# Kernel tuning notes

Hardware: AMD Instinct MI355X
Metric: run time of the kernel (lower is better)

Reference implementation:

```python
import jax, jax.numpy as jnp
import numpy as np

NUM_HEADS = 16
HEAD_DIM = 64
PATCH_NUMS = [1, 2, 3, 4, 5, 6, 8, 10, 13, 16, 32]
MAX_SCALE_MUL = float(np.log(100.0))


def precompute_freqs_cis(dim, patch_nums, theta=10000.0):
    # Returns [L, dim//2, 2] (cos, sin) pairs; matches torch.polar construction.
    freqs = 1.0 / theta ** (np.arange(0, dim, 4)[: dim // 4].astype(np.float32) / dim)  # [dim//4]
    tx, ty = [], []
    grid = 32.0
    for p in patch_nums:
        ix, iy = np.meshgrid(np.arange(p), np.arange(p), indexing="ij")  # torch default 'ij'
        tx.append(ix.flatten().astype(np.float32) / p * grid)
        ty.append(iy.flatten().astype(np.float32) / p * grid)
    tx = np.concatenate(tx)
    ty = np.concatenate(ty)
    ang = np.concatenate([np.outer(tx, freqs), np.outer(ty, freqs)], axis=1).astype(np.float32)  # [L, dim//2]
    return np.stack([np.cos(ang), np.sin(ang)], axis=-1)  # [L, dim//2, 2]


FREQS_CIS_CROSS = jnp.asarray(precompute_freqs_cis(HEAD_DIM, [12]))  # [144, 32, 2]


def _rope(x, cis):
    # x: [B, H, S, D]; cis: [S, D//2, 2] -> complex multiply on (even, odd) pairs.
    B, H, S, D = x.shape
    xr = x.reshape(B, H, S, D // 2, 2)
    a, b = xr[..., 0], xr[..., 1]
    c = cis[..., 0][None, None]  # [1,1,S,D//2]
    d = cis[..., 1][None, None]
    return jnp.stack([a * c - b * d, a * d + b * c], axis=-1).reshape(B, H, S, D)


def setup_inputs() -> dict:
    key = jax.random.key(0)
    ks = jax.random.split(key, 6)
    B, C, Ck, Lk = 8, 1024, 1024, 144
    fc = precompute_freqs_cis(HEAD_DIM, PATCH_NUMS)
    L = fc.shape[0]  # 1704
    return {
        "x": jax.random.normal(ks[0], (B, L, C), jnp.float32),
        "y": jax.random.normal(ks[1], (B, Lk, Ck), jnp.float32),
        "freqs_cis": jnp.asarray(fc),
        "attn_bias": jax.random.normal(ks[2], (1, 1, L, Lk), jnp.float32) * 0.1,
        "Wq": jax.random.normal(ks[3], (C, C), jnp.float32) * 0.02,
        "q_bias": jnp.zeros((C,), jnp.float32),
        "Wkv": jax.random.normal(ks[4], (2 * C, Ck), jnp.float32) * 0.02,
        "v_bias": jnp.zeros((C,), jnp.float32),
        "Wproj": jax.random.normal(ks[5], (C, C), jnp.float32) * 0.02,
        "b_proj": jnp.zeros((C,), jnp.float32),
        "scale_mul": jnp.full((1, NUM_HEADS, 1, 1), np.log(4.0), jnp.float32),
    }


def reference(x, y, freqs_cis, attn_bias, Wq, q_bias, Wkv, v_bias, Wproj, b_proj, scale_mul):
    B, L, C = x.shape
    H, D = NUM_HEADS, HEAD_DIM
    Lk = y.shape[1]
    # fused QKV projections (k bias is the zero buffer)
    q = (x @ Wq.T + q_bias).reshape(B, L, H, D).transpose(0, 2, 1, 3)  # [B,H,L,D]
    kv_bias = jnp.concatenate([jnp.zeros_like(v_bias), v_bias])
    kv = (y @ Wkv.T + kv_bias).reshape(B, Lk, 2, H, D)
    k = kv[:, :, 0].transpose(0, 2, 1, 3)  # [B,H,Lk,D]
    v = kv[:, :, 1].transpose(0, 2, 1, 3)
    # attn_l2_norm path: scale = 1, per-head learned multiplier
    sm = jnp.exp(jnp.minimum(scale_mul, MAX_SCALE_MUL))  # [1,H,1,1]
    q = q / jnp.maximum(jnp.linalg.norm(q, axis=-1, keepdims=True), 1e-12) * sm
    k = k / jnp.maximum(jnp.linalg.norm(k, axis=-1, keepdims=True), 1e-12)
    # inline RoPE (cross freqs recomputed from 12x12 grid every forward in the original)
    q = _rope(q, freqs_cis)
    k = _rope(k, FREQS_CIS_CROSS)
    # manual (non-flash) masked attention, scale = 1 due to l2 norm
    logits = jnp.einsum("bhld,bhkd->bhlk", q, k) + attn_bias
    attn = jax.nn.softmax(logits, axis=-1)
    oup = jnp.einsum("bhlk,bhkd->bhld", attn, v).transpose(0, 2, 1, 3).reshape(B, L, C)
    return oup @ Wproj.T + b_proj
```

## Files before the change

### kernel.cpp

```cpp
#include <hip/hip_runtime.h>

using u16 = unsigned short;
using u32 = unsigned int;

typedef __bf16 bf16x8 __attribute__((ext_vector_type(8)));
typedef float  f32x4  __attribute__((ext_vector_type(4)));
typedef _Float16 f16;
typedef _Float16 f16x4 __attribute__((ext_vector_type(4)));
typedef _Float16 f16x8 __attribute__((ext_vector_type(8)));
typedef u16 u16x4 __attribute__((ext_vector_type(4)));

__device__ __forceinline__ float b2f(u16 u) { return __uint_as_float(((u32)u) << 16); }
__device__ __forceinline__ u16 f2b(float f) {
    u32 u = __float_as_uint(f);
    return (u16)((u + 0x7FFFu + ((u >> 16) & 1u)) >> 16);
}

__device__ __forceinline__ void async_cp16(void* lds, const void* g) {
    __builtin_amdgcn_global_load_lds(
        (const __attribute__((address_space(1))) u32*)g,
        (__attribute__((address_space(3))) u32*)lds, 16, 0, 0);
}

__device__ __forceinline__ void split4_store(const float* src, u16* hi, u16* lo, int i) {
    f32x4 v = reinterpret_cast<const f32x4*>(src)[i];
    u16x4 H, L;
#pragma unroll
    for (int j = 0; j < 4; j++) {
        u16 hb = f2b(v[j]);
        H[j] = hb;
        L[j] = f2b(v[j] - b2f(hb));
    }
    reinterpret_cast<u16x4*>(hi)[i] = H;
    reinterpret_cast<u16x4*>(lo)[i] = L;
}

__global__ __launch_bounds__(256) void prep(const float* __restrict__ x,
                                            const float* __restrict__ Wq,
                                            const float* __restrict__ Wp,
                                            u16* __restrict__ xhi, u16* __restrict__ xlo,
                                            u16* __restrict__ wqhi, u16* __restrict__ wqlo,
                                            f16* __restrict__ wph,
                                            int nx4, int nw4) {
    int i = blockIdx.x * 256 + threadIdx.x;
    if (i < nx4) {
        split4_store(x, xhi, xlo, i);
    } else if (i < nx4 + nw4) {
        split4_store(Wq, wqhi, wqlo, i - nx4);
    } else {
        int k = i - nx4 - nw4;
        if (k < nw4) {
            f32x4 v = reinterpret_cast<const f32x4*>(Wp)[k];
            f16x4 h = {(f16)v[0], (f16)v[1], (f16)v[2], (f16)v[3]};
            reinterpret_cast<f16x4*>(wph)[k] = h;
        }
    }
}

__device__ __forceinline__ void split8(f32x4 a0, f32x4 a1, bf16x8& hi, bf16x8& lo) {
    union { bf16x8 v; u16 s[8]; } H, L;
#pragma unroll
    for (int j = 0; j < 4; j++) {
        float f = a0[j]; u16 hb = f2b(f); H.s[j] = hb;     L.s[j] = f2b(f - b2f(hb));
        float g = a1[j]; u16 gb = f2b(g); H.s[4 + j] = gb; L.s[4 + j] = f2b(g - b2f(gb));
    }
    hi = H.v; lo = L.v;
}

__global__ __launch_bounds__(256) void gemm_q(const u16* __restrict__ xhi,
                                              const u16* __restrict__ xlo,
                                              const u16* __restrict__ whi,
                                              const u16* __restrict__ wlo,
                                              const float* __restrict__ qb,
                                              const float* __restrict__ fc,
                                              const float* __restrict__ smul,
                                              f16* __restrict__ qout) {
    const int K = 1024, L = 1704;
    __shared__ u16 xs[2][2][64][64];
    int tid = threadIdx.x;
    int lane = tid & 63, wv = tid >> 6;
    int mt = blockIdx.x >> 2;
    int hg = blockIdx.x & 3;
    int h  = hg * 4 + wv;
    int lr = lane & 15, quad = lane >> 4;
    long m0 = (long)mt * 64;

    int r0 = tid >> 3, c0 = tid & 7;
    int s1 = tid + 256;
    int r1 = s1 >> 3, c1 = s1 & 7;
    const u16* srch0 = xhi + (m0 + r0) * K + ((c0 ^ (r0 & 7)) * 8);
    const u16* srch1 = xhi + (m0 + r1) * K + ((c1 ^ (r1 & 7)) * 8);
    const u16* srcl0 = xlo + (m0 + r0) * K + ((c0 ^ (r0 & 7)) * 8);
    const u16* srcl1 = xlo + (m0 + r1) * K + ((c1 ^ (r1 & 7)) * 8);
    u16* dh[2][2]; u16* dl[2][2];
    dh[0][0] = &xs[0][0][r0][c0 * 8]; dh[0][1] = &xs[0][0][r1][c1 * 8];
    dh[1][0] = &xs[1][0][r0][c0 * 8]; dh[1][1] = &xs[1][0][r1][c1 * 8];
    dl[0][0] = &xs[0][1][r0][c0 * 8]; dl[0][1] = &xs[0][1][r1][c1 * 8];
    dl[1][0] = &xs[1][1][r0][c0 * 8]; dl[1][1] = &xs[1][1][r1][c1 * 8];

    const bf16x8* wh_p[4];
    const bf16x8* wl_p[4];
#pragma unroll
    for (int i = 0; i < 4; i++) {
        long woff = ((long)(h * 64 + i * 16 + lr)) * K;
        wh_p[i] = reinterpret_cast<const bf16x8*>(whi + woff) + quad;
        wl_p[i] = reinterpret_cast<const bf16x8*>(wlo + woff) + quad;
    }

    int sp0 = ((0 + quad) ^ (lr & 7)) * 8;
    int sp1 = ((4 + quad) ^ (lr & 7)) * 8;

    f32x4 acc[4][4] = {};

    async_cp16(dh[0][0], srch0); async_cp16(dh[0][1], srch1);
    async_cp16(dl[0][0], srcl0); async_cp16(dl[0][1], srcl1);
    __syncthreads();

    for (int c = 0; c < 16; c++) {
        if (c < 15) {
            int nb = (c + 1) & 1;
            int off = (c + 1) * 64;
            async_cp16(dh[nb][0], srch0 + off); async_cp16(dh[nb][1], srch1 + off);
            async_cp16(dl[nb][0], srcl0 + off); async_cp16(dl[nb][1], srcl1 + off);
        }
        int buf = c & 1;
#pragma unroll
        for (int s = 0; s < 2; s++) {
            int sp = s ? sp1 : sp0;
            bf16x8 AH[4], AL[4], WH[4], WL[4];
#pragma unroll
            for (int i = 0; i < 4; i++) {
                WH[i] = wh_p[i][c * 8 + s * 4];
                WL[i] = wl_p[i][c * 8 + s * 4];
            }
#pragma unroll
            for (int i = 0; i < 4; i++) {
                AH[i] = *reinterpret_cast<const bf16x8*>(&xs[buf][0][i * 16 + lr][sp]);
                AL[i] = *reinterpret_cast<const bf16x8*>(&xs[buf][1][i * 16 + lr][sp]);
            }
#pragma unroll
            for (int mi = 0; mi < 4; mi++)
#pragma unroll
                for (int ni = 0; ni < 4; ni++) {
                    acc[mi][ni] = __builtin_amdgcn_mfma_f32_16x16x32_bf16(AH[mi], WH[ni], acc[mi][ni], 0, 0, 0);
                    acc[mi][ni] = __builtin_amdgcn_mfma_f32_16x16x32_bf16(AL[mi], WH[ni], acc[mi][ni], 0, 0, 0);
                    acc[mi][ni] = __builtin_amdgcn_mfma_f32_16x16x32_bf16(AH[mi], WL[ni], acc[mi][ni], 0, 0, 0);
                }
        }
        __syncthreads();
    }

    float sm = __expf(fminf(smul[h], 4.6051702f));
#pragma unroll
    for (int mi = 0; mi < 4; mi++) {
#pragma unroll
        for (int r = 0; r < 4; r++) {
            long rowg = m0 + mi * 16 + quad * 4 + r;
            float v[4];
            float ss = 0.f;
#pragma unroll
            for (int ni = 0; ni < 4; ni++) {
                v[ni] = acc[mi][ni][r] + qb[h * 64 + ni * 16 + lr];
                ss += v[ni] * v[ni];
            }
            ss += __shfl_xor(ss, 1, 64); ss += __shfl_xor(ss, 2, 64);
            ss += __shfl_xor(ss, 4, 64); ss += __shfl_xor(ss, 8, 64);
            float inv = sm / fmaxf(sqrtf(ss), 1e-12f);
            int l = (int)(rowg % L);
            f16* orow = qout + rowg * 1024 + h * 64;
#pragma unroll
            for (int ni = 0; ni < 4; ni++) {
                float u = v[ni] * inv;
                int d = ni * 16 + lr;
                int j = d >> 1;
                float c = fc[(l * 32 + j) * 2];
                float s = fc[(l * 32 + j) * 2 + 1];
                float pr = __shfl_xor(u, 1, 64);
                float o = (lane & 1) ? (pr * s + u * c) : (u * c - pr * s);
                orow[d] = (f16)o;
            }
        }
    }
}

__constant__ double FREQS16[16] = {
    1.0, 0.5623413251903491, 0.31622776601683794, 0.17782794100389228,
    0.1, 0.05623413251903491, 0.03162277660168379, 0.017782794100389228,
    0.01, 0.005623413251903491, 0.0031622776601683794, 0.0017782794100389228,
    0.001, 0.0005623413251903491, 0.00031622776601683794, 0.00017782794100389228};

__global__ __launch_bounds__(256) void gemm_kv(const float* __restrict__ y,
                                               const float* __restrict__ Wkv,
                                               const float* __restrict__ vb,
                                               f16* __restrict__ khp,
                                               f16* __restrict__ klp,
                                               f16* __restrict__ vhp,
                                               f16* __restrict__ vlp) {
    const int K = 1024;
    int lane = threadIdx.x & 63, wv = threadIdx.x >> 6;
    int mt = blockIdx.x >> 3;
    int nt = (blockIdx.x & 7) * 4 + wv;
    int lr = lane & 15, quad = lane >> 4;
    long m0 = (long)mt * 64;

    const float* arow[4];
    const float* wrow[4];
#pragma unroll
    for (int i = 0; i < 4; i++) {
        arow[i] = y   + (m0 + i * 16 + lr) * K + quad * 8;
        wrow[i] = Wkv + ((long)(nt * 64 + i * 16 + lr)) * K + quad * 8;
    }

    f32x4 acc[4][4] = {};
    for (int ks = 0; ks < 32; ks++) {
        bf16x8 ah[4], al[4], wh[4], wl[4];
#pragma unroll
        for (int i = 0; i < 4; i++) {
            const float* ap = arow[i] + ks * 32;
            split8(*(const f32x4*)ap, *(const f32x4*)(ap + 4), ah[i], al[i]);
            const float* wp = wrow[i] + ks * 32;
            split8(*(const f32x4*)wp, *(const f32x4*)(wp + 4), wh[i], wl[i]);
        }
#pragma unroll
        for (int mi = 0; mi < 4; mi++)
#pragma unroll
            for (int ni = 0; ni < 4; ni++) {
                acc[mi][ni] = __builtin_amdgcn_mfma_f32_16x16x32_bf16(ah[mi], wh[ni], acc[mi][ni], 0, 0, 0);
                acc[mi][ni] = __builtin_amdgcn_mfma_f32_16x16x32_bf16(al[mi], wh[ni], acc[mi][ni], 0, 0, 0);
                acc[mi][ni] = __builtin_amdgcn_mfma_f32_16x16x32_bf16(ah[mi], wl[ni], acc[mi][ni], 0, 0, 0);
            }
    }

    bool isv = nt >= 16;
    int h = isv ? nt - 16 : nt;
#pragma unroll
    for (int mi = 0; mi < 4; mi++) {
#pragma unroll
        for (int r = 0; r < 4; r++) {
            long row = m0 + mi * 16 + quad * 4 + r;
            int b = (int)(row / 144), lk = (int)(row % 144);
            long bh = b * 16 + h;
            float v[4];
#pragma unroll
            for (int ni = 0; ni < 4; ni++)
                v[ni] = acc[mi][ni][r] + (isv ? vb[h * 64 + ni * 16 + lr] : 0.f);
            if (!isv) {
                float ss = v[0] * v[0] + v[1] * v[1] + v[2] * v[2] + v[3] * v[3];
                ss += __shfl_xor(ss, 1, 64); ss += __shfl_xor(ss, 2, 64);
                ss += __shfl_xor(ss, 4, 64); ss += __shfl_xor(ss, 8, 64);
                float inv = 1.f / fmaxf(sqrtf(ss), 1e-12f);
                f16* kh_row = khp + (bh * 144 + lk) * 64;
                f16* kl_row = klp + (bh * 144 + lk) * 64;
#pragma unroll
                for (int ni = 0; ni < 4; ni++) {
                    float u = v[ni] * inv;
                    int d = ni * 16 + lr;
                    int j = d >> 1;
                    int f = j & 15;
                    float tc = (j < 16) ? ((float)(lk / 12)) / 12.0f * 32.0f
                                        : ((float)(lk % 12)) / 12.0f * 32.0f;
                    float ang = (float)((double)tc * FREQS16[f]);
                    float c = cosf(ang), s = sinf(ang);
                    float pr = __shfl_xor(u, 1, 64);
                    float o = (lane & 1) ? (pr * s + u * c) : (u * c - pr * s);
                    f16 oh = (f16)o;
                    f16 ol = (f16)(o - (float)oh);
                    kh_row[d] = oh;
                    kl_row[d] = ol;
                }
            } else {
#pragma unroll
                for (int ni = 0; ni < 4; ni++) {
                    float val = v[ni];
                    int d = ni * 16 + lr;
                    f16 vh = (f16)val;
                    f16 vl = (f16)(val - (float)vh);
                    vhp[(bh * 64 + d) * 144 + lk] = vh;
                    vlp[(bh * 64 + d) * 144 + lk] = vl;
                }
            }
        }
    }
}

__global__ __launch_bounds__(256, 3) void attn(const f16* q,
                                               const f16* __restrict__ khp,
                                               const f16* __restrict__ klp,
                                               const f16* __restrict__ vhp,
                                               const f16* __restrict__ vlp,
                                               const float* __restrict__ abias,
                                               f16* aout) {
    const int L = 1704;
    __shared__ __align__(16) f16 ps[4][16][152];
    int tid = threadIdx.x;
    int lane = tid & 63, wv = tid >> 6;
    int lr = lane & 15, quad = lane >> 4;
    int ltile = blockIdx.x % 27;
    int bh = blockIdx.x / 27;
    int h = bh & 15, b = bh >> 4;
    int l0 = ltile * 64;
    int rows = min(64, L - l0);

    int rA = wv * 16 + lr;
    int rAc = min(rA, rows - 1);
    const f16* qrow = q + ((long)(b * L + l0 + rAc)) * 1024 + h * 64;
    f16x8 qa0 = *reinterpret_cast<const f16x8*>(qrow + quad * 8);
    f16x8 qa1 = *reinterpret_cast<const f16x8*>(qrow + 32 + quad * 8);

    const f16* khb = khp + (long)bh * (144 * 64);
    const f16* klb = klp + (long)bh * (144 * 64);

    f32x4 acc[9] = {};
#pragma unroll
    for (int t = 0; t < 9; t++) {
        const f16* k0 = khb + (t * 16 + lr) * 64 + quad * 8;
        const f16* k1 = klb + (t * 16 + lr) * 64 + quad * 8;
        f16x8 bh0 = *reinterpret_cast<const f16x8*>(k0);
        f16x8 bh1 = *reinterpret_cast<const f16x8*>(k0 + 32);
        f16x8 bl0 = *reinterpret_cast<const f16x8*>(k1);
        f16x8 bl1 = *reinterpret_cast<const f16x8*>(k1 + 32);
        acc[t] = __builtin_amdgcn_mfma_f32_16x16x32_f16(qa0, bh0, acc[t], 0, 0, 0);
        acc[t] = __builtin_amdgcn_mfma_f32_16x16x32_f16(qa1, bh1, acc[t], 0, 0, 0);
        acc[t] = __builtin_amdgcn_mfma_f32_16x16x32_f16(qa0, bl0, acc[t], 0, 0, 0);
        acc[t] = __builtin_amdgcn_mfma_f32_16x16x32_f16(qa1, bl1, acc[t], 0, 0, 0);
    }

    int rC = wv * 16 + quad * 4;
#pragma unroll
    for (int r = 0; r < 4; r++) {
        long lrow = (long)(l0 + min(rC + r, rows - 1)) * 144;
#pragma unroll
        for (int t = 0; t < 9; t++) acc[t][r] += abias[lrow + t * 16 + lr];
    }

#pragma unroll
    for (int r = 0; r < 4; r++) {
        float mx = acc[0][r];
#pragma unroll
        for (int t = 1; t < 9; t++) mx = fmaxf(mx, acc[t][r]);
        mx = fmaxf(mx, __shfl_xor(mx, 1, 64));
        mx = fmaxf(mx, __shfl_xor(mx, 2, 64));
        mx = fmaxf(mx, __shfl_xor(mx, 4, 64));
        mx = fmaxf(mx, __shfl_xor(mx, 8, 64));
        float s = 0.f;
#pragma unroll
        for (int t = 0; t < 9; t++) {
            float e = __expf(acc[t][r] - mx);
            acc[t][r] = e;
            s += e;
        }
        s += __shfl_xor(s, 1, 64);
        s += __shfl_xor(s, 2, 64);
        s += __shfl_xor(s, 4, 64);
        s += __shfl_xor(s, 8, 64);
        float inv = 1.0f / s;
#pragma unroll
        for (int t = 0; t < 9; t++)
            ps[wv][quad * 4 + r][t * 16 + lr] = (f16)(acc[t][r] * inv);
    }

    const f16* vhb = vhp + (long)bh * (64 * 144);
    const f16* vlb = vlp + (long)bh * (64 * 144);
    f32x4 oacc[4] = {};
#pragma unroll
    for (int ks = 0; ks < 5; ks++) {
        f16x8 pa = {0, 0, 0, 0, 0, 0, 0, 0};
        if (ks < 4 || quad < 2)
            pa = *reinterpret_cast<const f16x8*>(&ps[wv][lr][ks * 32 + quad * 8]);
#pragma unroll
        for (int n = 0; n < 4; n++) {
            f16x8 vh8 = {0, 0, 0, 0, 0, 0, 0, 0};
            f16x8 vl8 = {0, 0, 0, 0, 0, 0, 0, 0};
            if (ks < 4 || quad < 2) {
                const f16* vr  = vhb + (n * 16 + lr) * 144 + ks * 32 + quad * 8;
                const f16* vr2 = vlb + (n * 16 + lr) * 144 + ks * 32 + quad * 8;
                vh8 = *reinterpret_cast<const f16x8*>(vr);
                vl8 = *reinterpret_cast<const f16x8*>(vr2);
            }
            oacc[n] = __builtin_amdgcn_mfma_f32_16x16x32_f16(pa, vh8, oacc[n], 0, 0, 0);
            oacc[n] = __builtin_amdgcn_mfma_f32_16x16x32_f16(pa, vl8, oacc[n], 0, 0, 0);
        }
    }

    long ob = (long)(b * L + l0);
#pragma unroll
    for (int r = 0; r < 4; r++) {
        int rw = rC + r;
        if (rw < rows) {
            f16* ao = aout + (ob + rw) * 1024 + h * 64;
#pragma unroll
            for (int n = 0; n < 4; n++) ao[n * 16 + lr] = (f16)oacc[n][r];
        }
    }
}

__global__ __launch_bounds__(256) void gemm_proj(const f16* __restrict__ A,
                                                 const f16* __restrict__ Wh,
                                                 const float* __restrict__ bias,
                                                 float* __restrict__ out) {
    const int K = 1024;
    __shared__ f16 as[2][64][64];
    int tid = threadIdx.x;
    int lane = tid & 63, wv = tid >> 6;
    int mt = blockIdx.x >> 2;
    int cg = blockIdx.x & 3;
    int lr = lane & 15, quad = lane >> 4;
    long m0 = (long)mt * 64;
    long n0 = (long)cg * 256 + wv * 64;

    int r0 = tid >> 3, c0 = tid & 7;
    int s1i = tid + 256;
    int r1 = s1i >> 3, c1 = s1i & 7;
    const f16* srca0 = A + (m0 + r0) * K + ((c0 ^ (r0 & 7)) * 8);
    const f16* srca1 = A + (m0 + r1) * K + ((c1 ^ (r1 & 7)) * 8);
    f16* da[2][2];
    da[0][0] = &as[0][r0][c0 * 8]; da[0][1] = &as[0][r1][c1 * 8];
    da[1][0] = &as[1][r0][c0 * 8]; da[1][1] = &as[1][r1][c1 * 8];

    const f16x8* wrow[4];
#pragma unroll
    for (int i = 0; i < 4; i++)
        wrow[i] = reinterpret_cast<const f16x8*>(Wh + (n0 + i * 16 + lr) * K) + quad;

    int sp0 = ((0 + quad) ^ (lr & 7)) * 8;
    int sp1 = ((4 + quad) ^ (lr & 7)) * 8;

    f32x4 acc[4][4] = {};

    async_cp16(da[0][0], srca0);
    async_cp16(da[0][1], srca1);
    __syncthreads();

    for (int c = 0; c < 16; c++) {
        if (c < 15) {
            int nb = (c + 1) & 1;
            int off = (c + 1) * 64;
            async_cp16(da[nb][0], srca0 + off);
            async_cp16(da[nb][1], srca1 + off);
        }
        int buf = c & 1;
#pragma unroll
        for (int s = 0; s < 2; s++) {
            int sp = s ? sp1 : sp0;
            f16x8 af[4], wf[4];
#pragma unroll
            for (int i = 0; i < 4; i++) wf[i] = wrow[i][c * 8 + s * 4];
#pragma unroll
            for (int i = 0; i < 4; i++)
                af[i] = *reinterpret_cast<const f16x8*>(&as[buf][i * 16 + lr][sp]);
#pragma unroll
            for (int mi = 0; mi < 4; mi++)
#pragma unroll
                for (int ni = 0; ni < 4; ni++)
                    acc[mi][ni] = __builtin_amdgcn_mfma_f32_16x16x32_f16(af[mi], wf[ni], acc[mi][ni], 0, 0, 0);
        }
        __syncthreads();
    }

#pragma unroll
    for (int ni = 0; ni < 4; ni++) {
        int col = (int)n0 + ni * 16 + lr;
        float b = bias[col];
#pragma unroll
        for (int mi = 0; mi < 4; mi++) {
            long row = m0 + mi * 16 + quad * 4;
#pragma unroll
            for (int r = 0; r < 4; r++)
                out[(row + r) * 1024 + col] = acc[mi][ni][r] + b;
        }
    }
}

extern "C" void kernel_launch(void* const* d_in, const int* in_sizes, int n_in,
                              void* d_out, int out_size, void* d_ws, size_t ws_size,
                              hipStream_t stream) {
    const float* x     = (const float*)d_in[0];
    const float* y     = (const float*)d_in[1];
    const float* fc    = (const float*)d_in[2];
    const float* abias = (const float*)d_in[3];
    const float* Wq    = (const float*)d_in[4];
    const float* qb    = (const float*)d_in[5];
    const float* Wkv   = (const float*)d_in[6];
    const float* vb    = (const float*)d_in[7];
    const float* Wp    = (const float*)d_in[8];
    const float* bp    = (const float*)d_in[9];
    const float* smul  = (const float*)d_in[10];

    const long XN = 13959168L;
    const long WN = 1048576L;
    const long KVN = 1179648L;

    f16* qbuf  = (f16*)d_ws;
    u16* wq_hi = (u16*)(qbuf + XN);
    u16* wq_lo = wq_hi + WN;
    f16* wp_h  = (f16*)(wq_lo + WN);

    u16* x_hi = (u16*)d_out;
    u16* x_lo = x_hi + XN;
    f16* kh_p  = (f16*)d_out;
    f16* kl_p  = kh_p + KVN;
    f16* vth_p = kl_p + KVN;
    f16* vtl_p = vth_p + KVN;

    int nx4 = (int)(XN / 4);
    int nw4 = (int)(WN / 4);
    int prep_blocks = (nx4 + 2 * nw4) / 256;

    prep<<<dim3(prep_blocks), dim3(256), 0, stream>>>(x, Wq, Wp, x_hi, x_lo,
                                                      wq_hi, wq_lo, wp_h, nx4, nw4);
    gemm_q<<<dim3(852), dim3(256), 0, stream>>>(x_hi, x_lo, wq_hi, wq_lo, qb, fc, smul, qbuf);
    gemm_kv<<<dim3(144), dim3(256), 0, stream>>>(y, Wkv, vb, kh_p, kl_p, vth_p, vtl_p);
    attn<<<dim3(3456), dim3(256), 0, stream>>>(qbuf, kh_p, kl_p, vth_p, vtl_p, abias, (f16*)qbuf);
    gemm_proj<<<dim3(852), dim3(256), 0, stream>>>((const f16*)qbuf, wp_h, bp, (float*)d_out);
}
```

Baseline: 586.2 us.

## Drop LDS staging in Q and proj GEMMs, load operands directly, remap blocks

Both GEMM kernels stop staging the activation tile through shared memory with async copies and barriers. Each wave now loads its A fragments straight from global memory, just like the weight fragments. Block indices are remapped so that groups of 8 consecutive M-tiles share a head or column group, which should help L2 reuse. Launch bounds also add occupancy hints (3 and 4 blocks). Without LDS, the 4 waves of a block load the same A rows redundantly, so the kernels depend more on cache hits and global latency and lose the double-buffered prefetch.

```diff
diff --git a/kernel.cpp b/kernel.cpp
--- a/kernel.cpp
+++ b/kernel.cpp
@@ -14,12 +14,6 @@
 __device__ __forceinline__ u16 f2b(float f) {
     u32 u = __float_as_uint(f);
     return (u16)((u + 0x7FFFu + ((u >> 16) & 1u)) >> 16);
-}
-
-__device__ __forceinline__ void async_cp16(void* lds, const void* g) {
-    __builtin_amdgcn_global_load_lds(
-        (const __attribute__((address_space(1))) u32*)g,
-        (__attribute__((address_space(3))) u32*)lds, 16, 0, 0);
 }
 
 __device__ __forceinline__ void split4_store(const float* src, u16* hi, u16* lo, int i) {
@@ -67,76 +61,62 @@
     hi = H.v; lo = L.v;
 }
 
-__global__ __launch_bounds__(256) void gemm_q(const u16* __restrict__ xhi,
-                                              const u16* __restrict__ xlo,
-                                              const u16* __restrict__ whi,
-                                              const u16* __restrict__ wlo,
-                                              const float* __restrict__ qb,
-                                              const float* __restrict__ fc,
-                                              const float* __restrict__ smul,
-                                              f16* __restrict__ qout) {
+__device__ __forceinline__ void remap852(int j, int& mt, int& sg) {
+    if (j < 832) {
+        int a = j >> 5, rem = j & 31;
+        mt = a * 8 + (rem & 7);
+        sg = rem >> 3;
+    } else {
+        int rem = j - 832;
+        mt = 208 + rem % 5;
+        sg = rem / 5;
+    }
+}
+
+__global__ __launch_bounds__(256, 3) void gemm_q(const u16* __restrict__ xhi,
+                                                 const u16* __restrict__ xlo,
+                                                 const u16* __restrict__ whi,
+                                                 const u16* __restrict__ wlo,
+                                                 const float* __restrict__ qb,
+                                                 const float* __restrict__ fc,
+                                                 const float* __restrict__ smul,
+                                                 f16* __restrict__ qout) {
     const int K = 1024, L = 1704;
-    __shared__ u16 xs[2][2][64][64];
     int tid = threadIdx.x;
     int lane = tid & 63, wv = tid >> 6;
-    int mt = blockIdx.x >> 2;
-    int hg = blockIdx.x & 3;
+    int mt, hg;
+    remap852(blockIdx.x, mt, hg);
     int h  = hg * 4 + wv;
     int lr = lane & 15, quad = lane >> 4;
     long m0 = (long)mt * 64;
 
-    int r0 = tid >> 3, c0 = tid & 7;
-    int s1 = tid + 256;
-    int r1 = s1 >> 3, c1 = s1 & 7;
-    const u16* srch0 = xhi + (m0 + r0) * K + ((c0 ^ (r0 & 7)) * 8);
-    const u16* srch1 = xhi + (m0 + r1) * K + ((c1 ^ (r1 & 7)) * 8);
-    const u16* srcl0 = xlo + (m0 + r0) * K + ((c0 ^ (r0 & 7)) * 8);
-    const u16* srcl1 = xlo + (m0 + r1) * K + ((c1 ^ (r1 & 7)) * 8);
-    u16* dh[2][2]; u16* dl[2][2];
-    dh[0][0] = &xs[0][0][r0][c0 * 8]; dh[0][1] = &xs[0][0][r1][c1 * 8];
-    dh[1][0] = &xs[1][0][r0][c0 * 8]; dh[1][1] = &xs[1][0][r1][c1 * 8];
-    dl[0][0] = &xs[0][1][r0][c0 * 8]; dl[0][1] = &xs[0][1][r1][c1 * 8];
-    dl[1][0] = &xs[1][1][r0][c0 * 8]; dl[1][1] = &xs[1][1][r1][c1 * 8];
-
+    const bf16x8* ah_p[4];
+    const bf16x8* al_p[4];
     const bf16x8* wh_p[4];
     const bf16x8* wl_p[4];
 #pragma unroll
     for (int i = 0; i < 4; i++) {
+        long aoff = (m0 + i * 16 + lr) * K;
+        ah_p[i] = reinterpret_cast<const bf16x8*>(xhi + aoff) + quad;
+        al_p[i] = reinterpret_cast<const bf16x8*>(xlo + aoff) + quad;
         long woff = ((long)(h * 64 + i * 16 + lr)) * K;
         wh_p[i] = reinterpret_cast<const bf16x8*>(whi + woff) + quad;
         wl_p[i] = reinterpret_cast<const bf16x8*>(wlo + woff) + quad;
     }
 
-    int sp0 = ((0 + quad) ^ (lr & 7)) * 8;
-    int sp1 = ((4 + quad) ^ (lr & 7)) * 8;
-
     f32x4 acc[4][4] = {};
 
-    async_cp16(dh[0][0], srch0); async_cp16(dh[0][1], srch1);
-    async_cp16(dl[0][0], srcl0); async_cp16(dl[0][1], srcl1);
-    __syncthreads();
-
     for (int c = 0; c < 16; c++) {
-        if (c < 15) {
-            int nb = (c + 1) & 1;
-            int off = (c + 1) * 64;
-            async_cp16(dh[nb][0], srch0 + off); async_cp16(dh[nb][1], srch1 + off);
-            async_cp16(dl[nb][0], srcl0 + off); async_cp16(dl[nb][1], srcl1 + off);
-        }
-        int buf = c & 1;
 #pragma unroll
         for (int s = 0; s < 2; s++) {
-            int sp = s ? sp1 : sp0;
+            int o = c * 8 + s * 4;
             bf16x8 AH[4], AL[4], WH[4], WL[4];
 #pragma unroll
             for (int i = 0; i < 4; i++) {
-                WH[i] = wh_p[i][c * 8 + s * 4];
-                WL[i] = wl_p[i][c * 8 + s * 4];
-            }
-#pragma unroll
-            for (int i = 0; i < 4; i++) {
-                AH[i] = *reinterpret_cast<const bf16x8*>(&xs[buf][0][i * 16 + lr][sp]);
-                AL[i] = *reinterpret_cast<const bf16x8*>(&xs[buf][1][i * 16 + lr][sp]);
+                WH[i] = wh_p[i][o];
+                WL[i] = wl_p[i][o];
+                AH[i] = ah_p[i][o];
+                AL[i] = al_p[i][o];
             }
 #pragma unroll
             for (int mi = 0; mi < 4; mi++)
@@ -147,7 +127,6 @@
                     acc[mi][ni] = __builtin_amdgcn_mfma_f32_16x16x32_bf16(AH[mi], WL[ni], acc[mi][ni], 0, 0, 0);
                 }
         }
-        __syncthreads();
     }
 
     float sm = __expf(fminf(smul[h], 4.6051702f));
@@ -394,67 +373,45 @@
     }
 }
 
-__global__ __launch_bounds__(256) void gemm_proj(const f16* __restrict__ A,
-                                                 const f16* __restrict__ Wh,
-                                                 const float* __restrict__ bias,
-                                                 float* __restrict__ out) {
+__global__ __launch_bounds__(256, 4) void gemm_proj(const f16* __restrict__ A,
+                                                    const f16* __restrict__ Wh,
+                                                    const float* __restrict__ bias,
+                                                    float* __restrict__ out) {
     const int K = 1024;
-    __shared__ f16 as[2][64][64];
     int tid = threadIdx.x;
     int lane = tid & 63, wv = tid >> 6;
-    int mt = blockIdx.x >> 2;
-    int cg = blockIdx.x & 3;
+    int mt, cg;
+    remap852(blockIdx.x, mt, cg);
     int lr = lane & 15, quad = lane >> 4;
     long m0 = (long)mt * 64;
     long n0 = (long)cg * 256 + wv * 64;
 
-    int r0 = tid >> 3, c0 = tid & 7;
-    int s1i = tid + 256;
-    int r1 = s1i >> 3, c1 = s1i & 7;
-    const f16* srca0 = A + (m0 + r0) * K + ((c0 ^ (r0 & 7)) * 8);
-    const f16* srca1 = A + (m0 + r1) * K + ((c1 ^ (r1 & 7)) * 8);
-    f16* da[2][2];
-    da[0][0] = &as[0][r0][c0 * 8]; da[0][1] = &as[0][r1][c1 * 8];
-    da[1][0] = &as[1][r0][c0 * 8]; da[1][1] = &as[1][r1][c1 * 8];
-
+    const f16x8* arow[4];
     const f16x8* wrow[4];
 #pragma unroll
-    for (int i = 0; i < 4; i++)
+    for (int i = 0; i < 4; i++) {
+        arow[i] = reinterpret_cast<const f16x8*>(A + (m0 + i * 16 + lr) * K) + quad;
         wrow[i] = reinterpret_cast<const f16x8*>(Wh + (n0 + i * 16 + lr) * K) + quad;
-
-    int sp0 = ((0 + quad) ^ (lr & 7)) * 8;
-    int sp1 = ((4 + quad) ^ (lr & 7)) * 8;
+    }
 
     f32x4 acc[4][4] = {};
 
-    async_cp16(da[0][0], srca0);
-    async_cp16(da[0][1], srca1);
-    __syncthreads();
-
     for (int c = 0; c < 16; c++) {
-        if (c < 15) {
-            int nb = (c + 1) & 1;
-            int off = (c + 1) * 64;
-            async_cp16(da[nb][0], srca0 + off);
-            async_cp16(da[nb][1], srca1 + off);
-        }
-        int buf = c & 1;
 #pragma unroll
         for (int s = 0; s < 2; s++) {
-            int sp = s ? sp1 : sp0;
+            int o = c * 8 + s * 4;
             f16x8 af[4], wf[4];
 #pragma unroll
-            for (int i = 0; i < 4; i++) wf[i] = wrow[i][c * 8 + s * 4];
-#pragma unroll
-            for (int i = 0; i < 4; i++)
-                af[i] = *reinterpret_cast<const f16x8*>(&as[buf][i * 16 + lr][sp]);
+            for (int i = 0; i < 4; i++) {
+                wf[i] = wrow[i][o];
+                af[i] = arow[i][o];
+            }
 #pragma unroll
             for (int mi = 0; mi < 4; mi++)
 #pragma unroll
                 for (int ni = 0; ni < 4; ni++)
                     acc[mi][ni] = __builtin_amdgcn_mfma_f32_16x16x32_f16(af[mi], wf[ni], acc[mi][ni], 0, 0, 0);
         }
-        __syncthreads();
     }
 
 #pragma unroll
```

New measurement: 732.1 us. 1.25x slower.
